# Kernel optimization log

Hardware: AMD Instinct MI355X
Metric: run time of the kernel (lower is better)

## Reference

```python
import jax, jax.numpy as jnp
import numpy as np

B, CLIP, P, E, H = 1024, 1024, 32, 2048, 16  # batch, clip_dim, prefix_length, token_emb_dim, num_heads
DH = E // H  # head dim = 128


def setup_inputs() -> dict:
    key = jax.random.key(0)
    ks = jax.random.split(key, 8)
    w = lambda k, sh: (jax.random.normal(k, sh, jnp.float32) * 0.02)
    return {
        "image_embs": jax.random.normal(ks[0], (B, CLIP), jnp.float32),
        "Wm": w(ks[1], (E, CLIP)),           # memory_proj weight
        "bm": jnp.zeros((E,), jnp.float32),
        "prefix_queries": w(ks[2], (P, E)),   # learned prefix queries
        "Win": w(ks[3], (3 * E, E)),          # MHA packed in_proj weight [q;k;v]
        "bin": jnp.zeros((3 * E,), jnp.float32),
        "Wo_mha": w(ks[4], (E, E)),           # MHA out_proj
        "bo_mha": jnp.zeros((E,), jnp.float32),
        "Wo": w(ks[5], (E, E)),               # adapter out_proj
        "bo": jnp.zeros((E,), jnp.float32),
    }


def reference(image_embs, Wm, bm, prefix_queries, Win, bin, Wo_mha, bo_mha, Wo, bo):
    Bn = image_embs.shape[0]
    # memory_proj: (B, clip_dim) -> (B, E); memory seq length is 1
    mem = image_embs @ Wm.T + bm
    # packed q/k/v projections, as in nn.MultiheadAttention
    Wq, Wk, Wv = Win[:E], Win[E:2 * E], Win[2 * E:]
    bq, bk, bv = bin[:E], bin[E:2 * E], bin[2 * E:]
    q = prefix_queries @ Wq.T + bq          # (P, E), shared across batch (queries are expanded)
    k = mem @ Wk.T + bk                     # (B, E)
    v = mem @ Wv.T + bv                     # (B, E)
    qh = q.reshape(P, H, DH)                # (P, H, dh)
    kh = k.reshape(Bn, H, DH)               # (B, H, dh)
    vh = v.reshape(Bn, H, DH)               # (B, H, dh)
    # scaled dot-product attention with kv_len = 1
    scores = jnp.einsum("phd,bhd->bhp", qh, kh) / jnp.sqrt(jnp.float32(DH))  # (B, H, P)
    attn = jax.nn.softmax(scores[..., None], axis=-1)  # (B, H, P, 1); trivially all-ones
    attn_out = jnp.einsum("bhpk,bhkd->bphd", attn, vh[:, :, None, :])  # (B, P, H, dh)
    attn_out = attn_out.reshape(Bn, P, E)
    out = attn_out @ Wo_mha.T + bo_mha      # MHA out_proj
    out = out @ Wo.T + bo                   # adapter out_proj
    return out
```

## Files before the change

kernel.cpp:

```cpp
#include <hip/hip_runtime.h>


#define BM 128
#define BN 64
#define BK 64
#define NBUF 4

typedef __attribute__((ext_vector_type(8))) __bf16 bf16x8;
typedef __attribute__((ext_vector_type(4))) float f32x4;

__device__ __forceinline__ unsigned short f2bf(float f) {
  unsigned int u = __float_as_uint(f);
  u += 0x7FFFu + ((u >> 16) & 1u);
  return (unsigned short)(u >> 16);
}

__global__ void cvt_all(const float* __restrict__ s0, const float* __restrict__ s1,
                        const float* __restrict__ s2, const float* __restrict__ s3,
                        const float* __restrict__ s4, unsigned short* __restrict__ dst) {
  const size_t NF4 = 3932160;
  size_t i = (size_t)blockIdx.x * blockDim.x + threadIdx.x;
  const size_t stride = (size_t)gridDim.x * blockDim.x;
  for (; i < NF4; i += stride) {
    const float* src; size_t off;
    if (i < 262144)       { src = s0; off = i; }
    else if (i < 786432)  { src = s1; off = i - 262144; }
    else if (i < 1835008) { src = s2; off = i - 786432; }
    else if (i < 2883584) { src = s3; off = i - 1835008; }
    else                  { src = s4; off = i - 2883584; }
    const float4 v = reinterpret_cast<const float4*>(src)[off];
    ushort4 o;
    o.x = f2bf(v.x); o.y = f2bf(v.y); o.z = f2bf(v.z); o.w = f2bf(v.w);
    reinterpret_cast<ushort4*>(dst)[i] = o;
  }
}

__device__ __forceinline__ void gload_lds16(const void* g, void* l) {
  __builtin_amdgcn_global_load_lds(
      (const __attribute__((address_space(1))) void*)g,
      (__attribute__((address_space(3))) void*)l, 16, 0, 0);
}

template <int EPI>
__global__ __launch_bounds__(256, 1) void gemm_bt(
    const unsigned short* __restrict__ A, const unsigned short* __restrict__ W,
    const float* __restrict__ bias, void* __restrict__ outp,
    int M, int N, int K) {
  __shared__ __attribute__((aligned(16))) unsigned short As[NBUF][BM * BK];
  __shared__ __attribute__((aligned(16))) unsigned short Bs[NBUF][BN * BK];
  const int tid = threadIdx.x;
  const int lane = tid & 63;
  const int wid = tid >> 6;
  const int wm = wid >> 1;
  const int wn = wid & 1;
  const int bid = blockIdx.x;
  const int bm0 = (bid & 7) * BM;
  const int bn0 = (bid >> 3) * BN;
  const int l15 = lane & 15;
  const int l4 = lane >> 4;
  const int lr = lane >> 3;
  const int lc = lane & 7;
  const int scol = ((lc ^ lr) << 3);

  f32x4 acc[4][2] = {};
  const size_t Kz = (size_t)K;

  auto stage = [&](int buf, int tile) {
    const int k0 = tile * BK;
#pragma unroll
    for (int j = 0; j < 4; ++j) {
      const int c = wid * 4 + j;
      gload_lds16(A + (size_t)(bm0 + c * 8 + lr) * Kz + (k0 + scol),
                  &As[buf][c * 512]);
    }
#pragma unroll
    for (int j = 0; j < 2; ++j) {
      const int c = wid * 2 + j;
      gload_lds16(W + (size_t)(bn0 + c * 8 + lr) * Kz + (k0 + scol),
                  &Bs[buf][c * 512]);
    }
  };

  auto compute = [&](int buf) {
    const int swz = (l15 & 7) << 3;
#pragma unroll
    for (int ks = 0; ks < 2; ++ks) {
      const int kidx = (ks * 32 + l4 * 8) ^ swz;
      bf16x8 a[4], b[2];
#pragma unroll
      for (int mi = 0; mi < 4; ++mi)
        a[mi] = *reinterpret_cast<const bf16x8*>(
            &As[buf][(wm * 64 + mi * 16 + l15) * 64 + kidx]);
#pragma unroll
      for (int ni = 0; ni < 2; ++ni)
        b[ni] = *reinterpret_cast<const bf16x8*>(
            &Bs[buf][(wn * 32 + ni * 16 + l15) * 64 + kidx]);
#pragma unroll
      for (int mi = 0; mi < 4; ++mi)
#pragma unroll
        for (int ni = 0; ni < 2; ++ni)
          acc[mi][ni] = __builtin_amdgcn_mfma_f32_16x16x32_bf16(
              a[mi], b[ni], acc[mi][ni], 0, 0, 0);
    }
  };

  const int nt = K >> 6;
  stage(0, 0); stage(1, 1); stage(2, 2);
  int t = 0;
  for (; t < nt - 3; ++t) {
    stage((t + 3) & 3, t + 3);
    asm volatile("s_waitcnt vmcnt(18)" ::: "memory");
    __builtin_amdgcn_s_barrier();
    compute(t & 3);
    __builtin_amdgcn_s_barrier();
  }
  asm volatile("s_waitcnt vmcnt(12)" ::: "memory");
  __builtin_amdgcn_s_barrier();
  compute(t & 3); ++t;
  __builtin_amdgcn_s_barrier();
  asm volatile("s_waitcnt vmcnt(6)" ::: "memory");
  __builtin_amdgcn_s_barrier();
  compute(t & 3); ++t;
  __builtin_amdgcn_s_barrier();
  asm volatile("s_waitcnt vmcnt(0)" ::: "memory");
  __builtin_amdgcn_s_barrier();
  compute(t & 3);

#pragma unroll
  for (int mi = 0; mi < 4; ++mi)
#pragma unroll
    for (int ni = 0; ni < 2; ++ni) {
      const int col = bn0 + wn * 32 + ni * 16 + l15;
      const float bcol = bias[col];
#pragma unroll
      for (int i = 0; i < 4; ++i) {
        const int row = bm0 + wm * 64 + mi * 16 + l4 * 4 + i;
        const float v = acc[mi][ni][i] + bcol;
        if (EPI == 0) {
          ((unsigned short*)outp)[(size_t)row * N + col] = f2bf(v);
        } else {
          ((float*)outp)[(size_t)row * N + col] = v;
        }
      }
    }
}

__global__ void bcast_rows(const f32x4* __restrict__ rowf, f32x4* __restrict__ out) {
  const size_t total = (size_t)1024 * 32 * 512;
  size_t i = (size_t)blockIdx.x * blockDim.x + threadIdx.x;
  const size_t stride = (size_t)gridDim.x * blockDim.x;
  for (; i < total; i += stride) {
    const size_t col4 = i & 511;
    const size_t b = i >> 14;
    const f32x4 v = rowf[(b << 9) | col4];
    __builtin_nontemporal_store(v, &out[i]);
  }
}

extern "C" void kernel_launch(void* const* d_in, const int* in_sizes, int n_in,
                              void* d_out, int out_size, void* d_ws, size_t ws_size,
                              hipStream_t stream) {
  const int CLIPd = 1024, Ed = 2048;
  const int Mb = in_sizes[0] / CLIPd;

  const float* image = (const float*)d_in[0];
  const float* bm   = (const float*)d_in[2];
  const float* Win  = (const float*)d_in[4];
  const float* bin  = (const float*)d_in[5];
  const float* bo1  = (const float*)d_in[7];
  const float* bo2  = (const float*)d_in[9];
  const float* Wm   = (const float*)d_in[1];
  const float* Wo1  = (const float*)d_in[6];
  const float* Wo2  = (const float*)d_in[8];
  float* out = (float*)d_out;

  unsigned short* wsb = (unsigned short*)d_ws;
  unsigned short* Xb   = wsb;
  unsigned short* Wmb  = wsb + (1u << 20);
  unsigned short* Wvb  = wsb + (3u << 20);
  unsigned short* W1b  = wsb + (7u << 20);
  unsigned short* W2b  = wsb + (11u << 20);
  unsigned short* act0 = wsb + (15u << 20);
  unsigned short* act1 = wsb + (17u << 20);
  unsigned short* act2 = wsb + (19u << 20);
  float* rowf = (float*)(wsb + (21u << 20));

  cvt_all<<<2048, 256, 0, stream>>>(image, Wm, Win + (size_t)2 * Ed * Ed,
                                    Wo1, Wo2, wsb);

  gemm_bt<0><<<256, 256, 0, stream>>>(Xb,   Wmb, bm,           act0, Mb, Ed, CLIPd);
  gemm_bt<0><<<256, 256, 0, stream>>>(act0, Wvb, bin + 2 * Ed, act1, Mb, Ed, Ed);
  gemm_bt<0><<<256, 256, 0, stream>>>(act1, W1b, bo1,          act2, Mb, Ed, Ed);
  gemm_bt<1><<<256, 256, 0, stream>>>(act2, W2b, bo2,          rowf, Mb, Ed, Ed);

  bcast_rows<<<4096, 256, 0, stream>>>((const f32x4*)rowf, (f32x4*)out);
  (void)n_in; (void)out_size; (void)ws_size;
}
```

Baseline: 164.1 us.

## Fuse all stages into one cooperative persistent kernel with grid syncs

Replaces the six separate launches (convert, four GEMMs, broadcast) with a single cooperative kernel of 256 blocks that runs each phase in turn, separated by grid-wide syncs. This removes per-launch overhead and the gaps between kernels. The GEMM main loop also drops one of its two barriers per tile by moving the wait and barrier ahead of the staging step. The broadcast is restructured so each block loads a row once and writes it 32 times. Tradeoffs: the convert phase now runs on only 256 blocks instead of 2048, and grid.sync adds its own cost.

```diff
diff --git a/kernel.cpp b/kernel.cpp
--- a/kernel.cpp
+++ b/kernel.cpp
@@ -1,4 +1,7 @@
 #include <hip/hip_runtime.h>
+#include <hip/hip_cooperative_groups.h>
+
+namespace cg = cooperative_groups;
 
 
 #define BM 128
@@ -15,13 +18,18 @@
   return (unsigned short)(u >> 16);
 }
 
-__global__ void cvt_all(const float* __restrict__ s0, const float* __restrict__ s1,
-                        const float* __restrict__ s2, const float* __restrict__ s3,
-                        const float* __restrict__ s4, unsigned short* __restrict__ dst) {
+__device__ __forceinline__ void gload_lds16(const void* g, void* l) {
+  __builtin_amdgcn_global_load_lds(
+      (const __attribute__((address_space(1))) void*)g,
+      (__attribute__((address_space(3))) void*)l, 16, 0, 0);
+}
+
+__device__ void cvt_phase(const float* __restrict__ s0, const float* __restrict__ s1,
+                          const float* __restrict__ s2, const float* __restrict__ s3,
+                          const float* __restrict__ s4, unsigned short* __restrict__ dst) {
   const size_t NF4 = 3932160;
   size_t i = (size_t)blockIdx.x * blockDim.x + threadIdx.x;
-  const size_t stride = (size_t)gridDim.x * blockDim.x;
-  for (; i < NF4; i += stride) {
+  for (; i < NF4; i += 65536) {
     const float* src; size_t off;
     if (i < 262144)       { src = s0; off = i; }
     else if (i < 786432)  { src = s1; off = i - 262144; }
@@ -35,19 +43,12 @@
   }
 }
 
-__device__ __forceinline__ void gload_lds16(const void* g, void* l) {
-  __builtin_amdgcn_global_load_lds(
-      (const __attribute__((address_space(1))) void*)g,
-      (__attribute__((address_space(3))) void*)l, 16, 0, 0);
-}
-
-template <int EPI>
-__global__ __launch_bounds__(256, 1) void gemm_bt(
-    const unsigned short* __restrict__ A, const unsigned short* __restrict__ W,
-    const float* __restrict__ bias, void* __restrict__ outp,
-    int M, int N, int K) {
-  __shared__ __attribute__((aligned(16))) unsigned short As[NBUF][BM * BK];
-  __shared__ __attribute__((aligned(16))) unsigned short Bs[NBUF][BN * BK];
+__device__ void gemm_phase(const unsigned short* __restrict__ A,
+                           const unsigned short* __restrict__ W,
+                           const float* __restrict__ bias,
+                           void* __restrict__ outp, int K, int EPI,
+                           unsigned short* __restrict__ As,
+                           unsigned short* __restrict__ Bs) {
   const int tid = threadIdx.x;
   const int lane = tid & 63;
   const int wid = tid >> 6;
@@ -61,9 +62,9 @@
   const int lr = lane >> 3;
   const int lc = lane & 7;
   const int scol = ((lc ^ lr) << 3);
+  const size_t Kz = (size_t)K;
 
   f32x4 acc[4][2] = {};
-  const size_t Kz = (size_t)K;
 
   auto stage = [&](int buf, int tile) {
     const int k0 = tile * BK;
@@ -71,17 +72,19 @@
     for (int j = 0; j < 4; ++j) {
       const int c = wid * 4 + j;
       gload_lds16(A + (size_t)(bm0 + c * 8 + lr) * Kz + (k0 + scol),
-                  &As[buf][c * 512]);
+                  As + buf * (BM * BK) + c * 512);
     }
 #pragma unroll
     for (int j = 0; j < 2; ++j) {
       const int c = wid * 2 + j;
       gload_lds16(W + (size_t)(bn0 + c * 8 + lr) * Kz + (k0 + scol),
-                  &Bs[buf][c * 512]);
+                  Bs + buf * (BN * BK) + c * 512);
     }
   };
 
   auto compute = [&](int buf) {
+    const unsigned short* Ab = As + buf * (BM * BK);
+    const unsigned short* Bb = Bs + buf * (BN * BK);
     const int swz = (l15 & 7) << 3;
 #pragma unroll
     for (int ks = 0; ks < 2; ++ks) {
@@ -90,11 +93,11 @@
 #pragma unroll
       for (int mi = 0; mi < 4; ++mi)
         a[mi] = *reinterpret_cast<const bf16x8*>(
-            &As[buf][(wm * 64 + mi * 16 + l15) * 64 + kidx]);
+            &Ab[(wm * 64 + mi * 16 + l15) * 64 + kidx]);
 #pragma unroll
       for (int ni = 0; ni < 2; ++ni)
         b[ni] = *reinterpret_cast<const bf16x8*>(
-            &Bs[buf][(wn * 32 + ni * 16 + l15) * 64 + kidx]);
+            &Bb[(wn * 32 + ni * 16 + l15) * 64 + kidx]);
 #pragma unroll
       for (int mi = 0; mi < 4; ++mi)
 #pragma unroll
@@ -108,20 +111,17 @@
   stage(0, 0); stage(1, 1); stage(2, 2);
   int t = 0;
   for (; t < nt - 3; ++t) {
+    asm volatile("s_waitcnt vmcnt(12)" ::: "memory");
+    __builtin_amdgcn_s_barrier();
     stage((t + 3) & 3, t + 3);
-    asm volatile("s_waitcnt vmcnt(18)" ::: "memory");
-    __builtin_amdgcn_s_barrier();
     compute(t & 3);
-    __builtin_amdgcn_s_barrier();
   }
   asm volatile("s_waitcnt vmcnt(12)" ::: "memory");
   __builtin_amdgcn_s_barrier();
   compute(t & 3); ++t;
-  __builtin_amdgcn_s_barrier();
   asm volatile("s_waitcnt vmcnt(6)" ::: "memory");
   __builtin_amdgcn_s_barrier();
   compute(t & 3); ++t;
-  __builtin_amdgcn_s_barrier();
   asm volatile("s_waitcnt vmcnt(0)" ::: "memory");
   __builtin_amdgcn_s_barrier();
   compute(t & 3);
@@ -136,45 +136,38 @@
       for (int i = 0; i < 4; ++i) {
         const int row = bm0 + wm * 64 + mi * 16 + l4 * 4 + i;
         const float v = acc[mi][ni][i] + bcol;
-        if (EPI == 0) {
-          ((unsigned short*)outp)[(size_t)row * N + col] = f2bf(v);
-        } else {
-          ((float*)outp)[(size_t)row * N + col] = v;
-        }
+        if (EPI == 0)
+          ((unsigned short*)outp)[(size_t)row * 2048 + col] = f2bf(v);
+        else
+          ((float*)outp)[(size_t)row * 2048 + col] = v;
       }
     }
 }
 
-__global__ void bcast_rows(const f32x4* __restrict__ rowf, f32x4* __restrict__ out) {
-  const size_t total = (size_t)1024 * 32 * 512;
-  size_t i = (size_t)blockIdx.x * blockDim.x + threadIdx.x;
-  const size_t stride = (size_t)gridDim.x * blockDim.x;
-  for (; i < total; i += stride) {
-    const size_t col4 = i & 511;
-    const size_t b = i >> 14;
-    const f32x4 v = rowf[(b << 9) | col4];
-    __builtin_nontemporal_store(v, &out[i]);
+__device__ void bcast_phase(const f32x4* __restrict__ rowf, f32x4* __restrict__ out) {
+  const int tid = threadIdx.x;
+  const int bid = blockIdx.x;
+#pragma unroll
+  for (int rb = 0; rb < 4; ++rb) {
+    const int b = bid * 4 + rb;
+    const f32x4 v0 = rowf[b * 512 + tid * 2];
+    const f32x4 v1 = rowf[b * 512 + tid * 2 + 1];
+    f32x4* ob = out + (size_t)b * 32 * 512;
+#pragma unroll 8
+    for (int p = 0; p < 32; ++p) {
+      __builtin_nontemporal_store(v0, &ob[p * 512 + tid * 2]);
+      __builtin_nontemporal_store(v1, &ob[p * 512 + tid * 2 + 1]);
+    }
   }
 }
 
-extern "C" void kernel_launch(void* const* d_in, const int* in_sizes, int n_in,
-                              void* d_out, int out_size, void* d_ws, size_t ws_size,
-                              hipStream_t stream) {
-  const int CLIPd = 1024, Ed = 2048;
-  const int Mb = in_sizes[0] / CLIPd;
-
-  const float* image = (const float*)d_in[0];
-  const float* bm   = (const float*)d_in[2];
-  const float* Win  = (const float*)d_in[4];
-  const float* bin  = (const float*)d_in[5];
-  const float* bo1  = (const float*)d_in[7];
-  const float* bo2  = (const float*)d_in[9];
-  const float* Wm   = (const float*)d_in[1];
-  const float* Wo1  = (const float*)d_in[6];
-  const float* Wo2  = (const float*)d_in[8];
-  float* out = (float*)d_out;
-
-  unsigned short* wsb = (unsigned short*)d_ws;
+__global__ __launch_bounds__(256, 1) void mega(
+    const float* image, const float* Wm, const float* bm_,
+    const float* Wv_f32, const float* bv_, const float* Wo1, const float* bo1,
+    const float* Wo2, const float* bo2, unsigned short* wsb, float* out) {
+  __shared__ __attribute__((aligned(16))) unsigned short As[NBUF * BM * BK];
+  __shared__ __attribute__((aligned(16))) unsigned short Bs[NBUF * BN * BK];
+
   unsigned short* Xb   = wsb;
   unsigned short* Wmb  = wsb + (1u << 20);
   unsigned short* Wvb  = wsb + (3u << 20);
@@ -185,14 +178,42 @@
   unsigned short* act2 = wsb + (19u << 20);
   float* rowf = (float*)(wsb + (21u << 20));
 
-  cvt_all<<<2048, 256, 0, stream>>>(image, Wm, Win + (size_t)2 * Ed * Ed,
-                                    Wo1, Wo2, wsb);
-
-  gemm_bt<0><<<256, 256, 0, stream>>>(Xb,   Wmb, bm,           act0, Mb, Ed, CLIPd);
-  gemm_bt<0><<<256, 256, 0, stream>>>(act0, Wvb, bin + 2 * Ed, act1, Mb, Ed, Ed);
-  gemm_bt<0><<<256, 256, 0, stream>>>(act1, W1b, bo1,          act2, Mb, Ed, Ed);
-  gemm_bt<1><<<256, 256, 0, stream>>>(act2, W2b, bo2,          rowf, Mb, Ed, Ed);
-
-  bcast_rows<<<4096, 256, 0, stream>>>((const f32x4*)rowf, (f32x4*)out);
-  (void)n_in; (void)out_size; (void)ws_size;
-}
+  cg::grid_group grid = cg::this_grid();
+
+  cvt_phase(image, Wm, Wv_f32, Wo1, Wo2, wsb);
+  grid.sync();
+  gemm_phase(Xb,   Wmb, bm_, act0, 1024, 0, As, Bs);
+  grid.sync();
+  gemm_phase(act0, Wvb, bv_, act1, 2048, 0, As, Bs);
+  grid.sync();
+  gemm_phase(act1, W1b, bo1, act2, 2048, 0, As, Bs);
+  grid.sync();
+  gemm_phase(act2, W2b, bo2, rowf, 2048, 1, As, Bs);
+  grid.sync();
+  bcast_phase((const f32x4*)rowf, (f32x4*)out);
+}
+
+extern "C" void kernel_launch(void* const* d_in, const int* in_sizes, int n_in,
+                              void* d_out, int out_size, void* d_ws, size_t ws_size,
+                              hipStream_t stream) {
+  const float* image = (const float*)d_in[0];
+  const float* Wm   = (const float*)d_in[1];
+  const float* bm   = (const float*)d_in[2];
+  const float* Win  = (const float*)d_in[4];
+  const float* bin  = (const float*)d_in[5];
+  const float* Wo1  = (const float*)d_in[6];
+  const float* bo1  = (const float*)d_in[7];
+  const float* Wo2  = (const float*)d_in[8];
+  const float* bo2  = (const float*)d_in[9];
+  float* out = (float*)d_out;
+
+  const float* Wv = Win + (size_t)2 * 2048 * 2048;
+  const float* bv = bin + 2 * 2048;
+  unsigned short* wsb = (unsigned short*)d_ws;
+
+  void* args[] = {(void*)&image, (void*)&Wm, (void*)&bm, (void*)&Wv, (void*)&bv,
+                  (void*)&Wo1, (void*)&bo1, (void*)&Wo2, (void*)&bo2,
+                  (void*)&wsb, (void*)&out};
+  hipLaunchCooperativeKernel((void*)mega, dim3(256), dim3(256), args, 0, stream);
+  (void)n_in; (void)in_sizes; (void)out_size; (void)ws_size;
+}
```

Measured after the change: 357.7 us. +118.0%, slower.

## Fuse next-layer weight conversion into GEMM tails and reorder pipeline barriers

Applied to the files above, without the earlier changes.

Splits the monolithic fp32-to-bf16 conversion so each GEMM converts the next layer's weight after its epilogue, which removes most of the separate conversion pass from the critical path. The GEMM main loop now uses a single barrier per K-step, waiting on vmcnt/lgkmcnt before issuing the next stage. Block-to-tile mapping is also changed to group N tiles differently, which may improve L2 reuse. The risk is that the tail conversion lengthens each GEMM and serializes with it rather than overlapping, and M/N are now hardcoded.

```diff
diff --git a/kernel.cpp b/kernel.cpp
--- a/kernel.cpp
+++ b/kernel.cpp
@@ -15,37 +15,32 @@
   return (unsigned short)(u >> 16);
 }
 
-__global__ void cvt_all(const float* __restrict__ s0, const float* __restrict__ s1,
-                        const float* __restrict__ s2, const float* __restrict__ s3,
-                        const float* __restrict__ s4, unsigned short* __restrict__ dst) {
-  const size_t NF4 = 3932160;
-  size_t i = (size_t)blockIdx.x * blockDim.x + threadIdx.x;
-  const size_t stride = (size_t)gridDim.x * blockDim.x;
-  for (; i < NF4; i += stride) {
-    const float* src; size_t off;
-    if (i < 262144)       { src = s0; off = i; }
-    else if (i < 786432)  { src = s1; off = i - 262144; }
-    else if (i < 1835008) { src = s2; off = i - 786432; }
-    else if (i < 2883584) { src = s3; off = i - 1835008; }
-    else                  { src = s4; off = i - 2883584; }
-    const float4 v = reinterpret_cast<const float4*>(src)[off];
-    ushort4 o;
-    o.x = f2bf(v.x); o.y = f2bf(v.y); o.z = f2bf(v.z); o.w = f2bf(v.w);
-    reinterpret_cast<ushort4*>(dst)[i] = o;
-  }
-}
-
 __device__ __forceinline__ void gload_lds16(const void* g, void* l) {
   __builtin_amdgcn_global_load_lds(
       (const __attribute__((address_space(1))) void*)g,
       (__attribute__((address_space(3))) void*)l, 16, 0, 0);
 }
 
-template <int EPI>
+__global__ __launch_bounds__(256) void cvt_xw(const float* __restrict__ x,
+                                              const float* __restrict__ wm,
+                                              unsigned short* __restrict__ dst) {
+  size_t i = (size_t)blockIdx.x * blockDim.x + threadIdx.x;
+  for (; i < 786432; i += 262144) {
+    const float4 v = (i < 262144)
+        ? reinterpret_cast<const float4*>(x)[i]
+        : reinterpret_cast<const float4*>(wm)[i - 262144];
+    ushort4 o;
+    o.x = f2bf(v.x); o.y = f2bf(v.y); o.z = f2bf(v.z); o.w = f2bf(v.w);
+    reinterpret_cast<ushort4*>(dst)[i] = o;
+  }
+}
+
+template <int EPI, bool CVT>
 __global__ __launch_bounds__(256, 1) void gemm_bt(
     const unsigned short* __restrict__ A, const unsigned short* __restrict__ W,
-    const float* __restrict__ bias, void* __restrict__ outp,
-    int M, int N, int K) {
+    const float* __restrict__ bias, void* __restrict__ outp, int K,
+    const float* __restrict__ cvt_src, unsigned short* __restrict__ cvt_dst,
+    int cvt_n4) {
   __shared__ __attribute__((aligned(16))) unsigned short As[NBUF][BM * BK];
   __shared__ __attribute__((aligned(16))) unsigned short Bs[NBUF][BN * BK];
   const int tid = threadIdx.x;
@@ -54,16 +49,16 @@
   const int wm = wid >> 1;
   const int wn = wid & 1;
   const int bid = blockIdx.x;
-  const int bm0 = (bid & 7) * BM;
-  const int bn0 = (bid >> 3) * BN;
+  const int bn0 = ((bid & 7) * 4 + (bid >> 6)) * BN;
+  const int bm0 = ((bid >> 3) & 7) * BM;
   const int l15 = lane & 15;
   const int l4 = lane >> 4;
   const int lr = lane >> 3;
   const int lc = lane & 7;
   const int scol = ((lc ^ lr) << 3);
+  const size_t Kz = (size_t)K;
 
   f32x4 acc[4][2] = {};
-  const size_t Kz = (size_t)K;
 
   auto stage = [&](int buf, int tile) {
     const int k0 = tile * BK;
@@ -108,21 +103,19 @@
   stage(0, 0); stage(1, 1); stage(2, 2);
   int t = 0;
   for (; t < nt - 3; ++t) {
+    asm volatile("s_waitcnt vmcnt(12)" ::: "memory");
+    asm volatile("s_waitcnt lgkmcnt(0)" ::: "memory");
+    __builtin_amdgcn_s_barrier();
     stage((t + 3) & 3, t + 3);
-    asm volatile("s_waitcnt vmcnt(18)" ::: "memory");
-    __builtin_amdgcn_s_barrier();
     compute(t & 3);
-    __builtin_amdgcn_s_barrier();
-  }
-  asm volatile("s_waitcnt vmcnt(12)" ::: "memory");
+  }
+  asm volatile("s_waitcnt vmcnt(12) lgkmcnt(0)" ::: "memory");
   __builtin_amdgcn_s_barrier();
   compute(t & 3); ++t;
-  __builtin_amdgcn_s_barrier();
-  asm volatile("s_waitcnt vmcnt(6)" ::: "memory");
+  asm volatile("s_waitcnt vmcnt(6) lgkmcnt(0)" ::: "memory");
   __builtin_amdgcn_s_barrier();
   compute(t & 3); ++t;
-  __builtin_amdgcn_s_barrier();
-  asm volatile("s_waitcnt vmcnt(0)" ::: "memory");
+  asm volatile("s_waitcnt vmcnt(0) lgkmcnt(0)" ::: "memory");
   __builtin_amdgcn_s_barrier();
   compute(t & 3);
 
@@ -136,16 +129,26 @@
       for (int i = 0; i < 4; ++i) {
         const int row = bm0 + wm * 64 + mi * 16 + l4 * 4 + i;
         const float v = acc[mi][ni][i] + bcol;
-        if (EPI == 0) {
-          ((unsigned short*)outp)[(size_t)row * N + col] = f2bf(v);
-        } else {
-          ((float*)outp)[(size_t)row * N + col] = v;
-        }
+        if (EPI == 0)
+          ((unsigned short*)outp)[(size_t)row * 2048 + col] = f2bf(v);
+        else
+          ((float*)outp)[(size_t)row * 2048 + col] = v;
       }
     }
-}
-
-__global__ void bcast_rows(const f32x4* __restrict__ rowf, f32x4* __restrict__ out) {
+
+  if (CVT) {
+    size_t i = (size_t)bid * 256 + tid;
+    for (; i < (size_t)cvt_n4; i += 65536) {
+      const float4 v = reinterpret_cast<const float4*>(cvt_src)[i];
+      ushort4 o;
+      o.x = f2bf(v.x); o.y = f2bf(v.y); o.z = f2bf(v.z); o.w = f2bf(v.w);
+      reinterpret_cast<ushort4*>(cvt_dst)[i] = o;
+    }
+  }
+}
+
+__global__ __launch_bounds__(256) void bcast_rows(const f32x4* __restrict__ rowf,
+                                                  f32x4* __restrict__ out) {
   const size_t total = (size_t)1024 * 32 * 512;
   size_t i = (size_t)blockIdx.x * blockDim.x + threadIdx.x;
   const size_t stride = (size_t)gridDim.x * blockDim.x;
@@ -160,19 +163,19 @@
 extern "C" void kernel_launch(void* const* d_in, const int* in_sizes, int n_in,
                               void* d_out, int out_size, void* d_ws, size_t ws_size,
                               hipStream_t stream) {
-  const int CLIPd = 1024, Ed = 2048;
-  const int Mb = in_sizes[0] / CLIPd;
-
   const float* image = (const float*)d_in[0];
+  const float* Wm   = (const float*)d_in[1];
   const float* bm   = (const float*)d_in[2];
   const float* Win  = (const float*)d_in[4];
   const float* bin  = (const float*)d_in[5];
+  const float* Wo1  = (const float*)d_in[6];
   const float* bo1  = (const float*)d_in[7];
+  const float* Wo2  = (const float*)d_in[8];
   const float* bo2  = (const float*)d_in[9];
-  const float* Wm   = (const float*)d_in[1];
-  const float* Wo1  = (const float*)d_in[6];
-  const float* Wo2  = (const float*)d_in[8];
   float* out = (float*)d_out;
+
+  const float* Wv = Win + (size_t)2 * 2048 * 2048;
+  const float* bv = bin + 2 * 2048;
 
   unsigned short* wsb = (unsigned short*)d_ws;
   unsigned short* Xb   = wsb;
@@ -185,14 +188,17 @@
   unsigned short* act2 = wsb + (19u << 20);
   float* rowf = (float*)(wsb + (21u << 20));
 
-  cvt_all<<<2048, 256, 0, stream>>>(image, Wm, Win + (size_t)2 * Ed * Ed,
-                                    Wo1, Wo2, wsb);
-
-  gemm_bt<0><<<256, 256, 0, stream>>>(Xb,   Wmb, bm,           act0, Mb, Ed, CLIPd);
-  gemm_bt<0><<<256, 256, 0, stream>>>(act0, Wvb, bin + 2 * Ed, act1, Mb, Ed, Ed);
-  gemm_bt<0><<<256, 256, 0, stream>>>(act1, W1b, bo1,          act2, Mb, Ed, Ed);
-  gemm_bt<1><<<256, 256, 0, stream>>>(act2, W2b, bo2,          rowf, Mb, Ed, Ed);
+  cvt_xw<<<1024, 256, 0, stream>>>(image, Wm, wsb);
+
+  gemm_bt<0, true><<<256, 256, 0, stream>>>(Xb, Wmb, bm, act0, 1024,
+                                            Wv, Wvb, 1048576);
+  gemm_bt<0, true><<<256, 256, 0, stream>>>(act0, Wvb, bv, act1, 2048,
+                                            Wo1, W1b, 1048576);
+  gemm_bt<0, true><<<256, 256, 0, stream>>>(act1, W1b, bo1, act2, 2048,
+                                            Wo2, W2b, 1048576);
+  gemm_bt<1, false><<<256, 256, 0, stream>>>(act2, W2b, bo2, rowf, 2048,
+                                             nullptr, nullptr, 0);
 
   bcast_rows<<<4096, 256, 0, stream>>>((const f32x4*)rowf, (f32x4*)out);
-  (void)n_in; (void)out_size; (void)ws_size;
-}
+  (void)n_in; (void)in_sizes; (void)out_size; (void)ws_size;
+}
```

Result: slower. 168.4 us (+2.6%).
